# Optimization experiments

Hardware: AMD Instinct MI355X
Metric: run time of the kernel (lower is better)

Reference implementation:

```python
import jax, jax.numpy as jnp
import numpy as np

SEG_LENS = [2048, 8192]
DIL_RATES = [1, 2]


def _dilated_attention(q, k, v, is_causal):
    # q,k,v: [b, n, h, d]
    b, n, h, d = q.shape
    ng = len(SEG_LENS)
    g = h // ng  # heads per group (even split)
    scale = 1.0 / np.sqrt(d).astype(np.float32)
    out = jnp.zeros_like(q)
    for i, (s, r) in enumerate(zip(SEG_LENS, DIL_RATES)):
        hs = i * g
        offset = i % r  # offset_idx % dilation_rate, as in _create_dilation_pattern
        idx = np.arange(offset, s, r)  # dilated positions within a segment, length m
        m = idx.shape[0]
        ns = n // s  # number of segments
        # reshape to segments then gather dilated positions: [b, ns, m, g, d]
        qg = q[:, :, hs:hs + g, :].reshape(b, ns, s, g, d)[:, :, idx]
        kg = k[:, :, hs:hs + g, :].reshape(b, ns, s, g, d)[:, :, idx]
        vg = v[:, :, hs:hs + g, :].reshape(b, ns, s, g, d)[:, :, idx]
        # segment-local attention over dilated tokens only (structured sparsity)
        scores = jnp.einsum('bsqhd,bskhd->bshqk', qg, kg) * scale
        if is_causal:
            cm = np.tril(np.ones((m, m), dtype=bool))  # idx is sorted -> causal in dilated order
            scores = jnp.where(cm, scores, -jnp.inf)
        attn = jax.nn.softmax(scores, axis=-1)
        og = jnp.einsum('bshqk,bskhd->bsqhd', attn, vg)  # [b, ns, m, g, d]
        # scatter back to full segment positions; non-dilated positions stay zero
        full = jnp.zeros((b, ns, s, g, d), q.dtype).at[:, :, idx].set(og)
        out = out.at[:, :, hs:hs + g, :].set(full.reshape(b, n, g, d))
    return out


def setup_inputs() -> dict:
    key = jax.random.key(0)
    k1, k2, k3 = jax.random.split(key, 3)
    shape = (1, 8192, 8, 64)
    q = jax.random.normal(k1, shape, dtype=jnp.float32)
    k = jax.random.normal(k2, shape, dtype=jnp.float32)
    v = jax.random.normal(k3, shape, dtype=jnp.float32)
    return {"q": q, "k": k, "v": v, "is_causal": 1}


def reference(q, k, v, is_causal):
    return _dilated_attention(q, k, v, bool(is_causal))
```

## Files before the change

### kernel.cpp

```cpp
#include <hip/hip_runtime.h>


#define LP 72

typedef __attribute__((ext_vector_type(8))) short bf16x8;
typedef __attribute__((ext_vector_type(4))) float f32x4;
typedef const unsigned int __attribute__((address_space(1)))* gp1;
typedef unsigned int __attribute__((address_space(3)))* lp3;

__device__ __forceinline__ unsigned short f2bf(float f) {
  unsigned u = __builtin_bit_cast(unsigned, f);
  u += 0x7fff + ((u >> 16) & 1);
  return (unsigned short)(u >> 16);
}

__device__ __forceinline__ int region_base(int head) {
  return (head < 4) ? head * 524288 : 2097152 + (head - 4) * 262144;
}

__device__ __forceinline__ void gl_lds16(const unsigned short* g, unsigned short* l) {
  __builtin_amdgcn_global_load_lds((gp1)g, (lp3)l, 16, 0, 0);
}

__global__ __launch_bounds__(256, 4)
void prep_kernel(const float* __restrict__ K, const float* __restrict__ V,
                 unsigned short* __restrict__ Kb, unsigned short* __restrict__ Vt) {
  __shared__ unsigned short sT[64][LP];
  const int bid = blockIdx.x;
  int head, pos0, rate, off;
  if (bid < 512) { head = bid >> 7; pos0 = (bid & 127) * 64; rate = 1; off = 0; }
  else { int b = bid - 512; head = 4 + (b >> 6); pos0 = (b & 63) * 64; rate = 2; off = 1; }
  const int rb = region_base(head);
  const int tid = threadIdx.x;
  const int row = tid >> 2, dg = tid & 3;
  const long tok = (long)(pos0 + row) * rate + off;

  {
    const float* kp = K + tok * 512 + head * 64 + dg * 16;
    unsigned short tmp[16];
    #pragma unroll
    for (int i = 0; i < 4; ++i) {
      float4 f = ((const float4*)kp)[i];
      tmp[i * 4 + 0] = f2bf(f.x); tmp[i * 4 + 1] = f2bf(f.y);
      tmp[i * 4 + 2] = f2bf(f.z); tmp[i * 4 + 3] = f2bf(f.w);
    }
    const int s = row & 7;
    unsigned short* dstrow = Kb + rb + (long)(pos0 + row) * 64;
    *(int4*)(dstrow + (((2 * dg)     ^ s) * 8)) = ((int4*)tmp)[0];
    *(int4*)(dstrow + (((2 * dg + 1) ^ s) * 8)) = ((int4*)tmp)[1];
  }

  {
    const float* vp = V + tok * 512 + head * 64 + dg * 16;
    #pragma unroll
    for (int i = 0; i < 4; ++i) {
      float4 f = ((const float4*)vp)[i];
      unsigned* p = (unsigned*)&sT[row][dg * 16 + i * 4];
      p[0] = (unsigned)f2bf(f.x) | ((unsigned)f2bf(f.y) << 16);
      p[1] = (unsigned)f2bf(f.z) | ((unsigned)f2bf(f.w) << 16);
    }
  }
  __syncthreads();

  {
    const int wv = tid >> 6, lane = tid & 63;
    unsigned pk[8];
    #pragma unroll
    for (int j = 0; j < 8; ++j) {
      unsigned lo = sT[wv * 16 + 2 * j][lane];
      unsigned hi = sT[wv * 16 + 2 * j + 1][lane];
      pk[j] = lo | (hi << 16);
    }
    const int s = lane & 7;
    unsigned short* dstrow = Vt + rb + (long)pos0 * 64 + lane * 64;
    int4 a = {(int)pk[0], (int)pk[1], (int)pk[2], (int)pk[3]};
    int4 b = {(int)pk[4], (int)pk[5], (int)pk[6], (int)pk[7]};
    *(int4*)(dstrow + (((2 * wv)     ^ s) * 8)) = a;
    *(int4*)(dstrow + (((2 * wv + 1) ^ s) * 8)) = b;
  }
}

__global__ __launch_bounds__(256, 2)
void attn_kernel(const float* __restrict__ Q, const unsigned short* __restrict__ Kb,
                 const unsigned short* __restrict__ Vt, const int* __restrict__ IC,
                 float* __restrict__ O, float* __restrict__ Slots) {
  __shared__ __attribute__((aligned(16))) unsigned short sK[2][4096];
  __shared__ __attribute__((aligned(16))) unsigned short sV[2][4096];
  __shared__ __attribute__((aligned(16))) unsigned short sP[4][1024];

  const int bid = blockIdx.x;
  int head, q0, seg0, mseg, rate, off, grp, chunk, slot;
  if (bid < 512) {
    int t = 63 - (bid >> 3);
    int h4 = (bid >> 1) & 3;
    head = 4 + h4; seg0 = 0; mseg = 4096;
    rate = 2; off = 1; grp = 1;
    q0 = t * 64;
    chunk = bid & 1;
    slot = (h4 * 64 + t) * 2 + chunk;
  } else {
    int cc = bid - 512;
    int t = cc >> 4;
    int job = cc & 15;
    head = job & 3;
    seg0 = (job >> 2) * 2048;
    q0 = seg0 + t * 64; mseg = 2048;
    rate = 1; off = 0; grp = 0; chunk = 0; slot = 0;
  }
  const int rb = region_base(head);
  const bool causal = (*IC) != 0;
  const int tid = threadIdx.x, wave = tid >> 6, lane = tid & 63;
  const int l16 = lane & 15, quad = lane >> 4;
  const int ch0 = ((quad ^ (l16 & 7)) * 8);
  const int ch1 = ch0 ^ 32;

  const int qloc = q0 - seg0;
  const int diagkb = qloc >> 6;
  const int nkb = causal ? diagkb + 1 : (mseg >> 6);
  const int klo = grp ? chunk * 32 : 0;
  const int khi = grp ? min(nkb, klo + 32) : nkb;
  if (klo >= khi) return;

  bf16x8 aQ[2];
  {
    long tok = (long)(q0 + wave * 16 + l16) * rate + off;
    const float* qp = Q + tok * 512 + head * 64 + quad * 8;
    #pragma unroll
    for (int kc = 0; kc < 2; ++kc) {
      float4 f0 = ((const float4*)(qp + kc * 32))[0];
      float4 f1 = ((const float4*)(qp + kc * 32))[1];
      bf16x8 a;
      a[0] = (short)f2bf(f0.x * 0.125f); a[1] = (short)f2bf(f0.y * 0.125f);
      a[2] = (short)f2bf(f0.z * 0.125f); a[3] = (short)f2bf(f0.w * 0.125f);
      a[4] = (short)f2bf(f1.x * 0.125f); a[5] = (short)f2bf(f1.y * 0.125f);
      a[6] = (short)f2bf(f1.z * 0.125f); a[7] = (short)f2bf(f1.w * 0.125f);
      aQ[kc] = a;
    }
  }

  f32x4 oacc[4], lacc;
  lacc = (f32x4){0.f, 0.f, 0.f, 0.f};
  #pragma unroll
  for (int dt = 0; dt < 4; ++dt) oacc[dt] = (f32x4){0.f, 0.f, 0.f, 0.f};
  bf16x8 vones;
  #pragma unroll
  for (int i = 0; i < 8; ++i) vones[i] = (short)0x3F80;

  unsigned short* myP = &sP[wave][0];
  const unsigned short* Ksrc = Kb + rb + (long)seg0 * 64;
  const unsigned short* Vsrc = Vt + rb + (long)seg0 * 64;

  const int o0 = wave * 1024;
  const int lo = lane * 8;
  {
    const unsigned short* kt = Ksrc + (long)klo * 4096;
    const unsigned short* vt = Vsrc + (long)klo * 4096;
    gl_lds16(kt + o0 + lo,       &sK[0][o0]);
    gl_lds16(kt + o0 + 512 + lo, &sK[0][o0 + 512]);
    gl_lds16(vt + o0 + lo,       &sV[0][o0]);
    gl_lds16(vt + o0 + 512 + lo, &sV[0][o0 + 512]);
  }

  for (int kb = klo; kb < khi; ++kb) {
    const int cur = (kb - klo) & 1;
    __syncthreads();
    if (kb + 1 < khi) {
      const unsigned short* kt = Ksrc + (long)(kb + 1) * 4096;
      const unsigned short* vt = Vsrc + (long)(kb + 1) * 4096;
      gl_lds16(kt + o0 + lo,       &sK[cur ^ 1][o0]);
      gl_lds16(kt + o0 + 512 + lo, &sK[cur ^ 1][o0 + 512]);
      gl_lds16(vt + o0 + lo,       &sV[cur ^ 1][o0]);
      gl_lds16(vt + o0 + 512 + lo, &sV[cur ^ 1][o0 + 512]);
    }
    const unsigned short* kbuf = &sK[cur][0];
    const unsigned short* vbuf = &sV[cur][0];

    f32x4 sc[4];
    #pragma unroll
    for (int c = 0; c < 4; ++c) {
      const unsigned short* krow = &kbuf[(c * 16 + l16) * 64];
      bf16x8 b0 = *(const bf16x8*)(krow + ch0);
      bf16x8 b1 = *(const bf16x8*)(krow + ch1);
      f32x4 z = (f32x4){0.f, 0.f, 0.f, 0.f};
      z = __builtin_amdgcn_mfma_f32_16x16x32_bf16(aQ[0], b0, z, 0, 0, 0);
      z = __builtin_amdgcn_mfma_f32_16x16x32_bf16(aQ[1], b1, z, 0, 0, 0);
      sc[c] = z;
    }

    const bool needMask = causal && (kb == diagkb);
    #pragma unroll
    for (int c = 0; c < 4; ++c) {
      #pragma unroll
      for (int r = 0; r < 4; ++r) {
        float e = __expf(sc[c][r]);
        if (needMask && (kb * 64 + c * 16 + l16 > qloc + wave * 16 + quad * 4 + r)) e = 0.f;
        const int qrow = quad * 4 + r;
        const int cidx = c * 2 + (l16 >> 3);
        myP[qrow * 64 + ((cidx ^ (qrow & 7)) << 3) + (l16 & 7)] = f2bf(e);
      }
    }
    const int swr = l16 & 7;
    bf16x8 aP0 = *(const bf16x8*)&myP[l16 * 64 + ((quad ^ swr) << 3)];
    bf16x8 aP1 = *(const bf16x8*)&myP[l16 * 64 + (((quad + 4) ^ swr) << 3)];
    lacc = __builtin_amdgcn_mfma_f32_16x16x32_bf16(aP0, vones, lacc, 0, 0, 0);
    lacc = __builtin_amdgcn_mfma_f32_16x16x32_bf16(aP1, vones, lacc, 0, 0, 0);

    #pragma unroll
    for (int dt = 0; dt < 4; ++dt) {
      const unsigned short* vrow = &vbuf[(dt * 16 + l16) * 64];
      bf16x8 v0 = *(const bf16x8*)(vrow + ch0);
      bf16x8 v1 = *(const bf16x8*)(vrow + ch1);
      oacc[dt] = __builtin_amdgcn_mfma_f32_16x16x32_bf16(aP0, v0, oacc[dt], 0, 0, 0);
      oacc[dt] = __builtin_amdgcn_mfma_f32_16x16x32_bf16(aP1, v1, oacc[dt], 0, 0, 0);
    }
  }

  if (grp == 1) {
    float* S = Slots + (long)slot * 4160;
    #pragma unroll
    for (int r = 0; r < 4; ++r) {
      int row = wave * 16 + quad * 4 + r;
      #pragma unroll
      for (int dt = 0; dt < 4; ++dt)
        S[row * 64 + dt * 16 + l16] = oacc[dt][r];
    }
    if (l16 == 0) {
      #pragma unroll
      for (int r = 0; r < 4; ++r)
        S[4096 + wave * 16 + quad * 4 + r] = lacc[r];
    }
  } else {
    #pragma unroll
    for (int r = 0; r < 4; ++r) {
      int tq = q0 + wave * 16 + quad * 4 + r;
      long tok = (long)tq * rate + off;
      float inv = 1.0f / lacc[r];
      float* dst = O + tok * 512 + head * 64 + l16;
      #pragma unroll
      for (int dt = 0; dt < 4; ++dt)
        dst[dt * 16] = oacc[dt][r] * inv;
    }
  }
}

__global__ __launch_bounds__(256, 4)
void combine_kernel(const float* __restrict__ Slots, const int* __restrict__ IC,
                    float* __restrict__ O) {
  const int b = blockIdx.x;
  const int h4 = b >> 6, t = b & 63;
  const bool causal = (*IC) != 0;
  const int nkb = causal ? t + 1 : 64;
  const int nc = (nkb > 32) ? 2 : 1;
  const float* s0 = Slots + (long)((h4 * 64 + t) * 2) * 4160;
  const int tid = threadIdx.x;
  const int row = tid >> 2, dq = (tid & 3) * 16;

  float4 acc[4];
  const float4* p0 = (const float4*)(s0 + row * 64 + dq);
  #pragma unroll
  for (int i = 0; i < 4; ++i) acc[i] = p0[i];
  float l = s0[4096 + row];
  if (nc == 2) {
    const float* s1 = s0 + 4160;
    const float4* p1 = (const float4*)(s1 + row * 64 + dq);
    #pragma unroll
    for (int i = 0; i < 4; ++i) {
      float4 v = p1[i];
      acc[i].x += v.x; acc[i].y += v.y; acc[i].z += v.z; acc[i].w += v.w;
    }
    l += s1[4096 + row];
  }
  const float inv = 1.0f / l;
  const long tok = (long)(t * 64 + row) * 2 + 1;
  float* dst = O + tok * 512 + (4 + h4) * 64 + dq;
  #pragma unroll
  for (int i = 0; i < 4; ++i) {
    float4 o = {acc[i].x * inv, acc[i].y * inv, acc[i].z * inv, acc[i].w * inv};
    ((float4*)dst)[i] = o;
  }
  float* dste = O + (tok - 1) * 512 + (4 + h4) * 64 + dq;
  const float4 z = {0.f, 0.f, 0.f, 0.f};
  #pragma unroll
  for (int i = 0; i < 4; ++i) ((float4*)dste)[i] = z;
}

extern "C" void kernel_launch(void* const* d_in, const int* in_sizes, int n_in,
                              void* d_out, int out_size, void* d_ws, size_t ws_size,
                              hipStream_t stream) {
  const float* q = (const float*)d_in[0];
  const float* k = (const float*)d_in[1];
  const float* v = (const float*)d_in[2];
  const int* ic = (const int*)d_in[3];
  unsigned short* Kb = (unsigned short*)d_ws;
  unsigned short* Vt = Kb + 3145728;
  float* Slots = (float*)((char*)d_ws + 12582912);
  prep_kernel<<<dim3(768), dim3(256), 0, stream>>>(k, v, Kb, Vt);
  attn_kernel<<<dim3(1024), dim3(256), 0, stream>>>(q, Kb, Vt, ic, (float*)d_out, Slots);
  combine_kernel<<<dim3(256), dim3(256), 0, stream>>>(Slots, ic, (float*)d_out);
}
```

Measured before the change: 145.5 us.

## Process two 64-row query tiles per block to reuse K/V tiles

Each attention block now handles 128 query rows (two 64-row sub-tiles) against the same staged K/V tiles, halving the grid and the combine grid. The aim is to halve global-to-LDS K/V traffic and per-block overhead. The cost is doubled accumulator registers, which can hurt occupancy under the 2-blocks launch bound. There is also fewer blocks for 256 CUs and some load imbalance, since the lower sub-tile skips work on the last diagonal block.

```diff
diff --git a/kernel.cpp b/kernel.cpp
--- a/kernel.cpp
+++ b/kernel.cpp
@@ -90,21 +90,22 @@
 
   const int bid = blockIdx.x;
   int head, q0, seg0, mseg, rate, off, grp, chunk, slot;
-  if (bid < 512) {
-    int t = 63 - (bid >> 3);
-    int h4 = (bid >> 1) & 3;
+  if (bid < 256) {
+    int g = bid >> 2;
+    int t = 31 - (g >> 1);
+    chunk = g & 1;
+    int h4 = bid & 3;
     head = 4 + h4; seg0 = 0; mseg = 4096;
     rate = 2; off = 1; grp = 1;
-    q0 = t * 64;
-    chunk = bid & 1;
-    slot = (h4 * 64 + t) * 2 + chunk;
+    q0 = t * 128;
+    slot = (h4 * 32 + t) * 2 + chunk;
   } else {
-    int cc = bid - 512;
+    int cc = bid - 256;
     int t = cc >> 4;
     int job = cc & 15;
     head = job & 3;
     seg0 = (job >> 2) * 2048;
-    q0 = seg0 + t * 64; mseg = 2048;
+    q0 = seg0 + t * 128; mseg = 2048;
     rate = 1; off = 0; grp = 0; chunk = 0; slot = 0;
   }
   const int rb = region_base(head);
@@ -115,15 +116,16 @@
   const int ch1 = ch0 ^ 32;
 
   const int qloc = q0 - seg0;
-  const int diagkb = qloc >> 6;
-  const int nkb = causal ? diagkb + 1 : (mseg >> 6);
+  const int diag0 = qloc >> 6;
+  const int nkb = causal ? diag0 + 2 : (mseg >> 6);
   const int klo = grp ? chunk * 32 : 0;
   const int khi = grp ? min(nkb, klo + 32) : nkb;
   if (klo >= khi) return;
 
-  bf16x8 aQ[2];
-  {
-    long tok = (long)(q0 + wave * 16 + l16) * rate + off;
+  bf16x8 aQ[2][2];
+  #pragma unroll
+  for (int rt = 0; rt < 2; ++rt) {
+    long tok = (long)(q0 + rt * 64 + wave * 16 + l16) * rate + off;
     const float* qp = Q + tok * 512 + head * 64 + quad * 8;
     #pragma unroll
     for (int kc = 0; kc < 2; ++kc) {
@@ -134,14 +136,17 @@
       a[2] = (short)f2bf(f0.z * 0.125f); a[3] = (short)f2bf(f0.w * 0.125f);
       a[4] = (short)f2bf(f1.x * 0.125f); a[5] = (short)f2bf(f1.y * 0.125f);
       a[6] = (short)f2bf(f1.z * 0.125f); a[7] = (short)f2bf(f1.w * 0.125f);
-      aQ[kc] = a;
-    }
-  }
-
-  f32x4 oacc[4], lacc;
-  lacc = (f32x4){0.f, 0.f, 0.f, 0.f};
-  #pragma unroll
-  for (int dt = 0; dt < 4; ++dt) oacc[dt] = (f32x4){0.f, 0.f, 0.f, 0.f};
+      aQ[rt][kc] = a;
+    }
+  }
+
+  f32x4 oacc[2][4], lacc[2];
+  #pragma unroll
+  for (int rt = 0; rt < 2; ++rt) {
+    lacc[rt] = (f32x4){0.f, 0.f, 0.f, 0.f};
+    #pragma unroll
+    for (int dt = 0; dt < 4; ++dt) oacc[rt][dt] = (f32x4){0.f, 0.f, 0.f, 0.f};
+  }
   bf16x8 vones;
   #pragma unroll
   for (int i = 0; i < 8; ++i) vones[i] = (short)0x3F80;
@@ -175,70 +180,96 @@
     const unsigned short* kbuf = &sK[cur][0];
     const unsigned short* vbuf = &sV[cur][0];
 
-    f32x4 sc[4];
+    const bool live0 = !causal || (kb <= diag0);
+
+    f32x4 sc[2][4];
     #pragma unroll
     for (int c = 0; c < 4; ++c) {
       const unsigned short* krow = &kbuf[(c * 16 + l16) * 64];
       bf16x8 b0 = *(const bf16x8*)(krow + ch0);
       bf16x8 b1 = *(const bf16x8*)(krow + ch1);
-      f32x4 z = (f32x4){0.f, 0.f, 0.f, 0.f};
-      z = __builtin_amdgcn_mfma_f32_16x16x32_bf16(aQ[0], b0, z, 0, 0, 0);
-      z = __builtin_amdgcn_mfma_f32_16x16x32_bf16(aQ[1], b1, z, 0, 0, 0);
-      sc[c] = z;
-    }
-
-    const bool needMask = causal && (kb == diagkb);
-    #pragma unroll
-    for (int c = 0; c < 4; ++c) {
+      f32x4 z1 = (f32x4){0.f, 0.f, 0.f, 0.f};
+      z1 = __builtin_amdgcn_mfma_f32_16x16x32_bf16(aQ[1][0], b0, z1, 0, 0, 0);
+      z1 = __builtin_amdgcn_mfma_f32_16x16x32_bf16(aQ[1][1], b1, z1, 0, 0, 0);
+      sc[1][c] = z1;
+      if (live0) {
+        f32x4 z0 = (f32x4){0.f, 0.f, 0.f, 0.f};
+        z0 = __builtin_amdgcn_mfma_f32_16x16x32_bf16(aQ[0][0], b0, z0, 0, 0, 0);
+        z0 = __builtin_amdgcn_mfma_f32_16x16x32_bf16(aQ[0][1], b1, z0, 0, 0, 0);
+        sc[0][c] = z0;
+      }
+    }
+
+    bf16x8 aP[2][2];
+    const int swr = l16 & 7;
+    #pragma unroll
+    for (int rt = 0; rt < 2; ++rt) {
+      if (rt == 0 && !live0) continue;
+      const bool needMask = causal && (kb == diag0 + rt);
       #pragma unroll
-      for (int r = 0; r < 4; ++r) {
-        float e = __expf(sc[c][r]);
-        if (needMask && (kb * 64 + c * 16 + l16 > qloc + wave * 16 + quad * 4 + r)) e = 0.f;
-        const int qrow = quad * 4 + r;
-        const int cidx = c * 2 + (l16 >> 3);
-        myP[qrow * 64 + ((cidx ^ (qrow & 7)) << 3) + (l16 & 7)] = f2bf(e);
-      }
-    }
-    const int swr = l16 & 7;
-    bf16x8 aP0 = *(const bf16x8*)&myP[l16 * 64 + ((quad ^ swr) << 3)];
-    bf16x8 aP1 = *(const bf16x8*)&myP[l16 * 64 + (((quad + 4) ^ swr) << 3)];
-    lacc = __builtin_amdgcn_mfma_f32_16x16x32_bf16(aP0, vones, lacc, 0, 0, 0);
-    lacc = __builtin_amdgcn_mfma_f32_16x16x32_bf16(aP1, vones, lacc, 0, 0, 0);
+      for (int c = 0; c < 4; ++c) {
+        #pragma unroll
+        for (int r = 0; r < 4; ++r) {
+          float e = __expf(sc[rt][c][r]);
+          if (needMask &&
+              (kb * 64 + c * 16 + l16 > qloc + rt * 64 + wave * 16 + quad * 4 + r)) e = 0.f;
+          const int qrow = quad * 4 + r;
+          const int cidx = c * 2 + (l16 >> 3);
+          myP[qrow * 64 + ((cidx ^ (qrow & 7)) << 3) + (l16 & 7)] = f2bf(e);
+        }
+      }
+      aP[rt][0] = *(const bf16x8*)&myP[l16 * 64 + ((quad ^ swr) << 3)];
+      aP[rt][1] = *(const bf16x8*)&myP[l16 * 64 + (((quad + 4) ^ swr) << 3)];
+      lacc[rt] = __builtin_amdgcn_mfma_f32_16x16x32_bf16(aP[rt][0], vones, lacc[rt], 0, 0, 0);
+      lacc[rt] = __builtin_amdgcn_mfma_f32_16x16x32_bf16(aP[rt][1], vones, lacc[rt], 0, 0, 0);
+    }
 
     #pragma unroll
     for (int dt = 0; dt < 4; ++dt) {
       const unsigned short* vrow = &vbuf[(dt * 16 + l16) * 64];
       bf16x8 v0 = *(const bf16x8*)(vrow + ch0);
       bf16x8 v1 = *(const bf16x8*)(vrow + ch1);
-      oacc[dt] = __builtin_amdgcn_mfma_f32_16x16x32_bf16(aP0, v0, oacc[dt], 0, 0, 0);
-      oacc[dt] = __builtin_amdgcn_mfma_f32_16x16x32_bf16(aP1, v1, oacc[dt], 0, 0, 0);
+      oacc[1][dt] = __builtin_amdgcn_mfma_f32_16x16x32_bf16(aP[1][0], v0, oacc[1][dt], 0, 0, 0);
+      oacc[1][dt] = __builtin_amdgcn_mfma_f32_16x16x32_bf16(aP[1][1], v1, oacc[1][dt], 0, 0, 0);
+      if (live0) {
+        oacc[0][dt] = __builtin_amdgcn_mfma_f32_16x16x32_bf16(aP[0][0], v0, oacc[0][dt], 0, 0, 0);
+        oacc[0][dt] = __builtin_amdgcn_mfma_f32_16x16x32_bf16(aP[0][1], v1, oacc[0][dt], 0, 0, 0);
+      }
     }
   }
 
   if (grp == 1) {
-    float* S = Slots + (long)slot * 4160;
-    #pragma unroll
-    for (int r = 0; r < 4; ++r) {
-      int row = wave * 16 + quad * 4 + r;
+    float* S = Slots + (long)slot * 8320;
+    #pragma unroll
+    for (int rt = 0; rt < 2; ++rt) {
       #pragma unroll
-      for (int dt = 0; dt < 4; ++dt)
-        S[row * 64 + dt * 16 + l16] = oacc[dt][r];
+      for (int r = 0; r < 4; ++r) {
+        int row = rt * 64 + wave * 16 + quad * 4 + r;
+        #pragma unroll
+        for (int dt = 0; dt < 4; ++dt)
+          S[row * 64 + dt * 16 + l16] = oacc[rt][dt][r];
+      }
     }
     if (l16 == 0) {
       #pragma unroll
-      for (int r = 0; r < 4; ++r)
-        S[4096 + wave * 16 + quad * 4 + r] = lacc[r];
+      for (int rt = 0; rt < 2; ++rt)
+        #pragma unroll
+        for (int r = 0; r < 4; ++r)
+          S[8192 + rt * 64 + wave * 16 + quad * 4 + r] = lacc[rt][r];
     }
   } else {
     #pragma unroll
-    for (int r = 0; r < 4; ++r) {
-      int tq = q0 + wave * 16 + quad * 4 + r;
-      long tok = (long)tq * rate + off;
-      float inv = 1.0f / lacc[r];
-      float* dst = O + tok * 512 + head * 64 + l16;
+    for (int rt = 0; rt < 2; ++rt) {
       #pragma unroll
-      for (int dt = 0; dt < 4; ++dt)
-        dst[dt * 16] = oacc[dt][r] * inv;
+      for (int r = 0; r < 4; ++r) {
+        int tq = q0 + rt * 64 + wave * 16 + quad * 4 + r;
+        long tok = (long)tq * rate + off;
+        float inv = 1.0f / lacc[rt][r];
+        float* dst = O + tok * 512 + head * 64 + l16;
+        #pragma unroll
+        for (int dt = 0; dt < 4; ++dt)
+          dst[dt * 16] = oacc[rt][dt][r] * inv;
+      }
     }
   }
 }
@@ -247,41 +278,41 @@
 void combine_kernel(const float* __restrict__ Slots, const int* __restrict__ IC,
                     float* __restrict__ O) {
   const int b = blockIdx.x;
-  const int h4 = b >> 6, t = b & 63;
+  const int h4 = b >> 5, t = b & 31;
   const bool causal = (*IC) != 0;
-  const int nkb = causal ? t + 1 : 64;
+  const int nkb = causal ? 2 * t + 2 : 64;
   const int nc = (nkb > 32) ? 2 : 1;
-  const float* s0 = Slots + (long)((h4 * 64 + t) * 2) * 4160;
+  const float* s0 = Slots + (long)((h4 * 32 + t) * 2) * 8320;
   const int tid = threadIdx.x;
-  const int row = tid >> 2, dq = (tid & 3) * 16;
-
-  float4 acc[4];
+  const int row = tid >> 1, dq = (tid & 1) * 32;
+
+  float4 acc[8];
   const float4* p0 = (const float4*)(s0 + row * 64 + dq);
   #pragma unroll
-  for (int i = 0; i < 4; ++i) acc[i] = p0[i];
-  float l = s0[4096 + row];
+  for (int i = 0; i < 8; ++i) acc[i] = p0[i];
+  float l = s0[8192 + row];
   if (nc == 2) {
-    const float* s1 = s0 + 4160;
+    const float* s1 = s0 + 8320;
     const float4* p1 = (const float4*)(s1 + row * 64 + dq);
     #pragma unroll
-    for (int i = 0; i < 4; ++i) {
+    for (int i = 0; i < 8; ++i) {
       float4 v = p1[i];
       acc[i].x += v.x; acc[i].y += v.y; acc[i].z += v.z; acc[i].w += v.w;
     }
-    l += s1[4096 + row];
+    l += s1[8192 + row];
   }
   const float inv = 1.0f / l;
-  const long tok = (long)(t * 64 + row) * 2 + 1;
+  const long tok = (long)(t * 128 + row) * 2 + 1;
   float* dst = O + tok * 512 + (4 + h4) * 64 + dq;
   #pragma unroll
-  for (int i = 0; i < 4; ++i) {
+  for (int i = 0; i < 8; ++i) {
     float4 o = {acc[i].x * inv, acc[i].y * inv, acc[i].z * inv, acc[i].w * inv};
     ((float4*)dst)[i] = o;
   }
   float* dste = O + (tok - 1) * 512 + (4 + h4) * 64 + dq;
   const float4 z = {0.f, 0.f, 0.f, 0.f};
   #pragma unroll
-  for (int i = 0; i < 4; ++i) ((float4*)dste)[i] = z;
+  for (int i = 0; i < 8; ++i) ((float4*)dste)[i] = z;
 }
 
 extern "C" void kernel_launch(void* const* d_in, const int* in_sizes, int n_in,
@@ -295,6 +326,6 @@
   unsigned short* Vt = Kb + 3145728;
   float* Slots = (float*)((char*)d_ws + 12582912);
   prep_kernel<<<dim3(768), dim3(256), 0, stream>>>(k, v, Kb, Vt);
-  attn_kernel<<<dim3(1024), dim3(256), 0, stream>>>(q, Kb, Vt, ic, (float*)d_out, Slots);
-  combine_kernel<<<dim3(256), dim3(256), 0, stream>>>(Slots, ic, (float*)d_out);
-}
+  attn_kernel<<<dim3(512), dim3(256), 0, stream>>>(q, Kb, Vt, ic, (float*)d_out, Slots);
+  combine_kernel<<<dim3(128), dim3(256), 0, stream>>>(Slots, ic, (float*)d_out);
+}
```

Result: slower. 161.1 us (+10.7%).
